# Optimization experiments

Hardware: AMD Instinct MI355X
Metric: run time of the kernel (lower is better)

## Reference

```python
import jax, jax.numpy as jnp
import numpy as np

B, LQ, LK, D, H = 2, 1024, 1024, 1024, 16
DH = D // H


def setup_inputs() -> dict:
    key = jax.random.key(0)
    ks = jax.random.split(key, 14)
    s = 1.0 / np.sqrt(D)
    inp = {
        "q": jax.random.normal(ks[0], (B, LQ, D), jnp.float32),
        "k": jax.random.normal(ks[1], (B, LK, D), jnp.float32),
        "v": jax.random.normal(ks[2], (B, LK, D), jnp.float32),
        "Wq": jax.random.normal(ks[3], (D, D), jnp.float32) * s,
        "bq": jnp.zeros((D,), jnp.float32),
        "Wk": jax.random.normal(ks[4], (D, D), jnp.float32) * s,
        "bk": jnp.zeros((D,), jnp.float32),
        "Wv": jax.random.normal(ks[5], (D, D), jnp.float32) * s,
        "bv": jnp.zeros((D,), jnp.float32),
        "Wo": jax.random.normal(ks[6], (D, D), jnp.float32) * s,
        "bo": jnp.zeros((D,), jnp.float32),
        "logits_bias": jax.random.normal(ks[7], (B, LQ, LK), jnp.float32),
        "key_padding_mask": jax.random.randint(ks[8], (B, LK), 0, 2) > 0,
    }
    return inp


def _split_heads(x):
    b, l, _ = x.shape
    return x.reshape(b, l, H, DH).transpose(0, 2, 1, 3)  # [B,H,L,DH]


def reference(q, k, v, Wq, bq, Wk, bk, Wv, bv, Wo, bo, logits_bias, key_padding_mask):
    qh = _split_heads(q @ Wq.T + bq)  # [B,H,Lq,DH]
    kh = _split_heads(k @ Wk.T + bk)  # [B,H,Lk,DH]
    vh = _split_heads(v @ Wv.T + bv)  # [B,H,Lk,DH]

    neg = jnp.finfo(qh.dtype).min
    # attn_mask = logits_bias broadcast over heads, masked_fill at padded keys
    attn_mask = jnp.where(key_padding_mask[:, None, None, :],
                          neg, logits_bias[:, None, :, :])  # [B,1,Lq,Lk]

    scale = 1.0 / np.sqrt(DH)
    scores = jnp.einsum('bhqd,bhkd->bhqk', qh, kh) * scale + attn_mask
    probs = jax.nn.softmax(scores, axis=-1)
    out = jnp.einsum('bhqk,bhkd->bhqd', probs, vh)  # [B,H,Lq,DH]
    out = out.transpose(0, 2, 1, 3).reshape(q.shape[0], q.shape[1], D)
    return out @ Wo.T + bo
```

## Files before the change

kernel.cpp:

```cpp
#include <hip/hip_runtime.h>


typedef _Float16 half8 __attribute__((ext_vector_type(8)));
typedef _Float16 half4_t __attribute__((ext_vector_type(4)));
typedef __fp16 fp16x2 __attribute__((ext_vector_type(2)));
typedef float f32x4 __attribute__((ext_vector_type(4)));
typedef unsigned int u32;

#define MFMA16(a, b, c) __builtin_amdgcn_mfma_f32_16x16x32_f16((a), (b), (c), 0, 0, 0)

#define WAITCNT_VM(n) asm volatile("s_waitcnt vmcnt(" #n ")" ::: "memory")
#define WAITCNT_LGKM0() asm volatile("s_waitcnt lgkmcnt(0)" ::: "memory")
#define RAW_BARRIER() asm volatile("s_barrier" ::: "memory")
#define EXP2F(x) __builtin_amdgcn_exp2f(x)

__device__ __forceinline__ void gload16(const void* g, void* l) {
  __builtin_amdgcn_global_load_lds(
      (const __attribute__((address_space(1))) unsigned int*)g,
      (__attribute__((address_space(3))) unsigned int*)l, 16, 0, 0);
}

__device__ __forceinline__ half8 frag_ld(const _Float16* t, int row, int ck) {
  return *(const half8*)(t + row * 64 + (((ck ^ (row & 7)) << 3)));
}

__global__ __launch_bounds__(256) void cvt_f32_f16(
    const float* __restrict__ q, const float* __restrict__ k, const float* __restrict__ v,
    const float* __restrict__ Wq, const float* __restrict__ Wk,
    const float* __restrict__ Wv, const float* __restrict__ Wo,
    _Float16* __restrict__ q16, _Float16* __restrict__ k16, _Float16* __restrict__ v16,
    _Float16* __restrict__ w16) {
  const int y = blockIdx.y;
  const float* s;
  _Float16* d;
  const size_t M = (size_t)1024 * 1024;
  int x = blockIdx.x;
  switch (y) {
    case 0: s = q;  d = q16; break;
    case 1: s = k;  d = k16; break;
    case 2: s = v;  d = v16; break;
    case 3: if (x < 512) { s = Wq; d = w16; } else { s = Wk; d = w16 + M; x -= 512; } break;
    default: if (x < 512) { s = Wv; d = w16 + 2 * M; } else { s = Wo; d = w16 + 3 * M; x -= 512; } break;
  }
  const size_t i = ((size_t)x * 256 + threadIdx.x) * 8;
  const float4 a = *(const float4*)(s + i);
  const float4 bvv = *(const float4*)(s + i + 4);
  half8 h;
  h[0] = (_Float16)a.x; h[1] = (_Float16)a.y; h[2] = (_Float16)a.z; h[3] = (_Float16)a.w;
  h[4] = (_Float16)bvv.x; h[5] = (_Float16)bvv.y; h[6] = (_Float16)bvv.z; h[7] = (_Float16)bvv.w;
  *(half8*)(d + i) = h;
}

__global__ __launch_bounds__(256, 2) void mmp_big(
    const _Float16* __restrict__ Aq, const _Float16* __restrict__ Ak,
    const _Float16* __restrict__ Av, const _Float16* __restrict__ W16,
    const float* __restrict__ c0, const float* __restrict__ c1,
    const float* __restrict__ c2, _Float16* __restrict__ Dq,
    _Float16* __restrict__ Dk, _Float16* __restrict__ Dvt) {
  __shared__ __align__(16) _Float16 lds[32768];

  const int tid = threadIdx.x;
  const int wv = tid >> 6, ln = tid & 63;
  const int quad = ln >> 4, col = ln & 15;
  const int wm = wv >> 1, wn = wv & 1;
  const int id = blockIdx.x;
  const int xcd = id & 7, idx = id >> 3;
  const int z = idx % 3;
  const int sub = idx / 3;
  const int n0 = ((xcd & 3) * 2 + (sub & 1)) * 128;
  const int m0 = ((xcd >> 2) * 8 + (sub >> 1)) * 128;
  const bool swapped = (z < 2);

  const _Float16* A = (z == 0) ? Aq : (z == 1) ? Ak : Av;
  const _Float16* Bw = W16 + (size_t)z * 1024 * 1024;
  const float* bias = (z == 0) ? c0 : (z == 1) ? c1 : c2;

  auto stage = [&](int buf, int k0) {
#pragma unroll
    for (int j = 0; j < 8; ++j) {
      const int ci = j * 256 + tid;
      const _Float16* src;
      if (ci < 1024) {
        const int row = ci >> 3, lc = (ci & 7) ^ (row & 7);
        src = A + (size_t)(m0 + row) * 1024 + k0 + lc * 8;
      } else {
        const int di = ci - 1024;
        const int row = di >> 3, lc = (di & 7) ^ (row & 7);
        src = Bw + (size_t)(n0 + row) * 1024 + k0 + lc * 8;
      }
      gload16(src, lds + buf * 16384 + (j * 256 + wv * 64) * 8);
    }
  };

  const f32x4 zero4 = {0.f, 0.f, 0.f, 0.f};
  f32x4 acc[4][4];
#pragma unroll
  for (int i = 0; i < 4; ++i)
#pragma unroll
    for (int j = 0; j < 4; ++j) acc[i][j] = zero4;

  auto kstep = [&](const _Float16* As, const _Float16* Bs) {
    half8 af0[4], bf0[4], af1[4], bf1[4];
#pragma unroll
    for (int mi = 0; mi < 4; ++mi) af0[mi] = frag_ld(As, wm * 64 + mi * 16 + col, quad);
#pragma unroll
    for (int ni = 0; ni < 4; ++ni) bf0[ni] = frag_ld(Bs, wn * 64 + ni * 16 + col, quad);
#pragma unroll
    for (int mi = 0; mi < 4; ++mi) af1[mi] = frag_ld(As, wm * 64 + mi * 16 + col, 4 + quad);
#pragma unroll
    for (int ni = 0; ni < 4; ++ni) bf1[ni] = frag_ld(Bs, wn * 64 + ni * 16 + col, 4 + quad);
    WAITCNT_LGKM0();
    RAW_BARRIER();
    if (swapped) {
#pragma unroll
      for (int ni = 0; ni < 4; ++ni)
#pragma unroll
        for (int mi = 0; mi < 4; ++mi)
          acc[ni][mi] = MFMA16(bf0[ni], af0[mi], acc[ni][mi]);
#pragma unroll
      for (int ni = 0; ni < 4; ++ni)
#pragma unroll
        for (int mi = 0; mi < 4; ++mi)
          acc[ni][mi] = MFMA16(bf1[ni], af1[mi], acc[ni][mi]);
    } else {
#pragma unroll
      for (int mi = 0; mi < 4; ++mi)
#pragma unroll
        for (int ni = 0; ni < 4; ++ni)
          acc[mi][ni] = MFMA16(af0[mi], bf0[ni], acc[mi][ni]);
#pragma unroll
      for (int mi = 0; mi < 4; ++mi)
#pragma unroll
        for (int ni = 0; ni < 4; ++ni)
          acc[mi][ni] = MFMA16(af1[mi], bf1[ni], acc[mi][ni]);
    }
  };

  stage(0, 0);
  for (int i = 0; i < 15; ++i) {
    stage((i + 1) & 1, (i + 1) * 64);
    WAITCNT_VM(8);
    RAW_BARRIER();
    kstep(lds + (i & 1) * 16384, lds + (i & 1) * 16384 + 8192);
  }
  WAITCNT_VM(0);
  RAW_BARRIER();
  kstep(lds + 16384, lds + 16384 + 8192);

  if (swapped) {
    float4 bv4[4];
#pragma unroll
    for (int ni = 0; ni < 4; ++ni)
      bv4[ni] = *(const float4*)&bias[n0 + wn * 64 + ni * 16 + quad * 4];
    _Float16* D = z ? Dk : Dq;
#pragma unroll
    for (int ni = 0; ni < 4; ++ni) {
      const int n_g = n0 + wn * 64 + ni * 16 + quad * 4;
      const int h = n_g >> 6, dh = n_g & 63;
#pragma unroll
      for (int mi = 0; mi < 4; ++mi) {
        const int m_g = m0 + wm * 64 + mi * 16 + col;
        const int b = m_g >> 10, l = m_g & 1023;
        half4_t st;
        st[0] = (_Float16)(acc[ni][mi][0] + bv4[ni].x);
        st[1] = (_Float16)(acc[ni][mi][1] + bv4[ni].y);
        st[2] = (_Float16)(acc[ni][mi][2] + bv4[ni].z);
        st[3] = (_Float16)(acc[ni][mi][3] + bv4[ni].w);
        *(half4_t*)&D[((size_t)((b * 16 + h) * 1024) + l) * 64 + dh] = st;
      }
    }
  } else {
    float bv[4];
#pragma unroll
    for (int ni = 0; ni < 4; ++ni) bv[ni] = bias[n0 + wn * 64 + ni * 16 + col];
    __syncthreads();
    _Float16* Ct = lds;
#pragma unroll
    for (int mi = 0; mi < 4; ++mi) {
      const int ml = wm * 64 + mi * 16 + quad * 4;
#pragma unroll
      for (int ni = 0; ni < 4; ++ni) {
        const int nl = wn * 64 + ni * 16 + col;
        half4_t h;
#pragma unroll
        for (int r = 0; r < 4; ++r) h[r] = (_Float16)(acc[mi][ni][r] + bv[ni]);
        *(half4_t*)(Ct + (size_t)nl * 136 + ml) = h;
      }
    }
    __syncthreads();
#pragma unroll
    for (int it = 0; it < 8; ++it) {
      const int ci = it * 256 + tid;
      const int n = ci >> 4;
      const int mc = (ci & 15) * 8;
      const half8 hv = *(const half8*)(Ct + (size_t)n * 136 + mc);
      const int n_g = n0 + n;
      const int h = n_g >> 6, dh = n_g & 63;
      const int m_g = m0 + mc;
      const int b = m_g >> 10, l = m_g & 1023;
      *(half8*)(Dvt + ((size_t)((b * 16 + h) * 64 + dh)) * 1024 + l) = hv;
    }
  }
}

__global__ __launch_bounds__(256) void mmp_final(
    const _Float16* __restrict__ A, const _Float16* __restrict__ Bw,
    const float* __restrict__ bias, float* __restrict__ Df) {
  __shared__ __align__(16) _Float16 lds[24576];

  const int tid = threadIdx.x;
  const int wv = tid >> 6, ln = tid & 63;
  const int quad = ln >> 4, col = ln & 15;
  const int wm = wv >> 1, wn = wv & 1;
  const int id = blockIdx.x;
  const int xcd = id & 7, idx = id >> 3;
  const int n0 = ((xcd & 1) * 4 + (idx & 3)) * 128;
  const int m0 = ((xcd >> 1) * 8 + (idx >> 2)) * 64;

  auto stage = [&](int buf, int k0) {
#pragma unroll
    for (int j = 0; j < 6; ++j) {
      const int ci = j * 256 + tid;
      const _Float16* src;
      if (ci < 512) {
        const int row = ci >> 3, lc = (ci & 7) ^ (row & 7);
        src = A + (size_t)(m0 + row) * 1024 + k0 + lc * 8;
      } else {
        const int di = ci - 512;
        const int row = di >> 3, lc = (di & 7) ^ (row & 7);
        src = Bw + (size_t)(n0 + row) * 1024 + k0 + lc * 8;
      }
      gload16(src, lds + buf * 12288 + (j * 256 + wv * 64) * 8);
    }
  };

  const f32x4 zero4 = {0.f, 0.f, 0.f, 0.f};
  f32x4 acc[4][2];
#pragma unroll
  for (int i = 0; i < 4; ++i)
#pragma unroll
    for (int j = 0; j < 2; ++j) acc[i][j] = zero4;

  auto kstep = [&](const _Float16* As, const _Float16* Bs) {
    half8 af[2][2], bf[2][4];
#pragma unroll
    for (int kk = 0; kk < 2; ++kk) {
#pragma unroll
      for (int mi = 0; mi < 2; ++mi)
        af[kk][mi] = frag_ld(As, wm * 32 + mi * 16 + col, kk * 4 + quad);
#pragma unroll
      for (int ni = 0; ni < 4; ++ni)
        bf[kk][ni] = frag_ld(Bs, wn * 64 + ni * 16 + col, kk * 4 + quad);
    }
    WAITCNT_LGKM0();
    RAW_BARRIER();
#pragma unroll
    for (int kk = 0; kk < 2; ++kk)
#pragma unroll
      for (int ni = 0; ni < 4; ++ni)
#pragma unroll
        for (int mi = 0; mi < 2; ++mi)
          acc[ni][mi] = MFMA16(bf[kk][ni], af[kk][mi], acc[ni][mi]);
  };

  stage(0, 0);
  for (int i = 0; i < 15; ++i) {
    stage((i + 1) & 1, (i + 1) * 64);
    WAITCNT_VM(6);
    RAW_BARRIER();
    kstep(lds + (i & 1) * 12288, lds + (i & 1) * 12288 + 4096);
  }
  WAITCNT_VM(0);
  RAW_BARRIER();
  kstep(lds + 12288, lds + 12288 + 4096);

  float4 bv4[4];
#pragma unroll
  for (int ni = 0; ni < 4; ++ni)
    bv4[ni] = *(const float4*)&bias[n0 + wn * 64 + ni * 16 + quad * 4];
#pragma unroll
  for (int ni = 0; ni < 4; ++ni) {
    const int n_g = n0 + wn * 64 + ni * 16 + quad * 4;
#pragma unroll
    for (int mi = 0; mi < 2; ++mi) {
      const int m_g = m0 + wm * 32 + mi * 16 + col;
      float4 st;
      st.x = acc[ni][mi][0] + bv4[ni].x;
      st.y = acc[ni][mi][1] + bv4[ni].y;
      st.z = acc[ni][mi][2] + bv4[ni].z;
      st.w = acc[ni][mi][3] + bv4[ni].w;
      *(float4*)&Df[(size_t)m_g * 1024 + n_g] = st;
    }
  }
}

__global__ __launch_bounds__(512, 4) void attn(
    const _Float16* __restrict__ Qh, const _Float16* __restrict__ Kh,
    const _Float16* __restrict__ Vt, const float* __restrict__ biasL,
    const int* __restrict__ kpm, _Float16* __restrict__ AO) {
  __shared__ __align__(16) _Float16 KV[3 * 8192];

  const int tid = threadIdx.x;
  const int wv = tid >> 6, ln = tid & 63;
  const int quad = ln >> 4, col = ln & 15;
  const int qsub = wv >> 1, khalf = wv & 1;
  const int fid = blockIdx.x;
  const int xcd = fid & 7, g = fid >> 3;
  const int bh = (xcd << 2) | (g >> 4);
  const int q0 = (g & 15) * 64;
  const int b = bh >> 4, hh = bh & 15;
  const int qg = q0 + qsub * 16 + col;

  const _Float16* Qp = Qh + ((size_t)bh * 1024 + qg) * 64;
  const half8 bq0 = *(const half8*)(Qp + quad * 8);
  const half8 bq1 = *(const half8*)(Qp + 32 + quad * 8);
  WAITCNT_VM(0);

  const float* biasRow = biasL + ((size_t)(b * 1024 + qg)) * 1024;
  const int* kpmRow = kpm + b * 1024;

  auto stageKV = [&](int buf, int it) {
    const int koff = it * 64;
#pragma unroll
    for (int j = 0; j < 2; ++j) {
      const int ci = j * 512 + tid;
      const void* src;
      if (ci < 512) {
        const int row = ci >> 3, lc = (ci & 7) ^ (row & 7);
        src = Kh + ((size_t)bh * 1024 + koff + row) * 64 + lc * 8;
      } else {
        const int di = ci - 512;
        const int row = di >> 3, lc = (di & 7) ^ (row & 7);
        src = Vt + ((size_t)bh * 64 + row) * 1024 + koff + lc * 8;
      }
      gload16(src, KV + buf * 8192 + (j * 512 + wv * 64) * 8);
    }
  };
  auto loadBias = [&](int it, f32x4* bb, int4* mk) {
    const int koff = it * 64 + khalf * 32;
#pragma unroll
    for (int mi = 0; mi < 2; ++mi) {
      const int kg = koff + mi * 16 + quad * 4;
      bb[mi] = *(const f32x4*)&biasRow[kg];
      mk[mi] = *(const int4*)&kpmRow[kg];
    }
  };

  const f32x4 zero4 = {0.f, 0.f, 0.f, 0.f};
  f32x4 o[4];
#pragma unroll
  for (int ni = 0; ni < 4; ++ni) o[ni] = zero4;
  float l_i = 0.f;

  auto pk = [](float a, float bb) -> u32 {
    union { fp16x2 h; u32 u; } cv;
    cv.h = __builtin_amdgcn_cvt_pkrtz(a, bb);
    return cv.u;
  };

  auto compute = [&](int buf, const f32x4* bb, const int4* mk) {
    const _Float16* Ks = KV + buf * 8192;
    const _Float16* Vs = Ks + 4096;
    f32x4 s[2];
#pragma unroll
    for (int mi = 0; mi < 2; ++mi) {
      f32x4 a4 = zero4;
      a4 = MFMA16(frag_ld(Ks, khalf * 32 + mi * 16 + col, quad), bq0, a4);
      a4 = MFMA16(frag_ld(Ks, khalf * 32 + mi * 16 + col, 4 + quad), bq1, a4);
      s[mi] = a4;
    }
#pragma unroll
    for (int mi = 0; mi < 2; ++mi) {
      const int* mp = (const int*)&mk[mi];
#pragma unroll
      for (int r = 0; r < 4; ++r) {
        const float sv = s[mi][r] * 0.18033688f + (bb[mi][r] * 1.44269504f - 8.f);
        const float p = mp[r] ? 0.f : EXP2F(sv);
        s[mi][r] = p;
        l_i += p;
      }
    }
    const u32 X0 = pk(s[0][0], s[0][1]), X1 = pk(s[0][2], s[0][3]);
    const u32 Y0 = pk(s[1][0], s[1][1]), Y1 = pk(s[1][2], s[1][3]);
    const u32 tX0 = __shfl_xor(X0, 16), tX1 = __shfl_xor(X1, 16);
    const u32 tY0 = __shfl_xor(Y0, 16), tY1 = __shfl_xor(Y1, 16);
    const bool e = (quad & 1) == 0;
    const u32 L0 = e ? X0 : tX0, L1 = e ? X1 : tX1, L2 = e ? tX0 : X0, L3 = e ? tX1 : X1;
    const u32 H0 = e ? Y0 : tY0, H1 = e ? Y1 : tY1, H2 = e ? tY0 : Y0, H3 = e ? tY1 : Y1;
    const bool lo2 = quad < 2;
    const u32 W0 = lo2 ? H0 : L0, W1 = lo2 ? H1 : L1, W2 = lo2 ? H2 : L2, W3 = lo2 ? H3 : L3;
    const u32 R0 = __shfl_xor(W0, 32), R1 = __shfl_xor(W1, 32);
    const u32 R2 = __shfl_xor(W2, 32), R3 = __shfl_xor(W3, 32);
    const bool mid = (quad == 1) || (quad == 2);
    union { u32 u[4]; half8 h; } pf;
    pf.u[0] = mid ? R0 : (lo2 ? L0 : H0);
    pf.u[1] = mid ? R1 : (lo2 ? L1 : H1);
    pf.u[2] = mid ? R2 : (lo2 ? L2 : H2);
    pf.u[3] = mid ? R3 : (lo2 ? L3 : H3);
#pragma unroll
    for (int ni = 0; ni < 4; ++ni)
      o[ni] = MFMA16(frag_ld(Vs, ni * 16 + col, khalf * 4 + quad), pf.h, o[ni]);
  };

  f32x4 bbA[2], bbB[2];
  int4 mkA[2], mkB[2];
  stageKV(0, 0);
  loadBias(0, bbA, mkA);
#pragma unroll 3
  for (int i = 0; i < 15; ++i) {
    stageKV((i + 1) % 3, i + 1);
    loadBias(i + 1, bbB, mkB);
    WAITCNT_VM(6);
    WAITCNT_LGKM0();
    RAW_BARRIER();
    compute(i % 3, bbA, mkA);
    bbA[0] = bbB[0]; bbA[1] = bbB[1];
    mkA[0] = mkB[0]; mkA[1] = mkB[1];
  }
  WAITCNT_VM(0);
  WAITCNT_LGKM0();
  RAW_BARRIER();
  compute(0, bbA, mkA);

  l_i += __shfl_xor(l_i, 16);
  l_i += __shfl_xor(l_i, 32);

  __syncthreads();
  f32x4* Ox = (f32x4*)&KV[0];
  float* MlS = (float*)&KV[8192];
  if (khalf == 1) {
#pragma unroll
    for (int ni = 0; ni < 4; ++ni) Ox[(qsub * 4 + ni) * 64 + ln] = o[ni];
    MlS[qsub * 64 + ln] = l_i;
  }
  __syncthreads();
  if (khalf == 0) {
    const float l2 = MlS[qsub * 64 + ln];
    const float inv = 1.0f / (l_i + l2);
#pragma unroll
    for (int ni = 0; ni < 4; ++ni) {
      const f32x4 o2 = Ox[(qsub * 4 + ni) * 64 + ln];
      half4_t h;
#pragma unroll
      for (int r = 0; r < 4; ++r)
        h[r] = (_Float16)((o[ni][r] + o2[r]) * inv);
      *(half4_t*)&AO[((size_t)(b * 1024 + qg)) * 1024 + hh * 64 + ni * 16 + quad * 4] = h;
    }
  }
}

extern "C" void kernel_launch(void* const* d_in, const int* in_sizes, int n_in,
                              void* d_out, int out_size, void* d_ws, size_t ws_size,
                              hipStream_t stream) {
  (void)in_sizes; (void)n_in; (void)out_size; (void)ws_size;
  const float* q = (const float*)d_in[0];
  const float* k = (const float*)d_in[1];
  const float* v = (const float*)d_in[2];
  const float* Wq = (const float*)d_in[3];
  const float* bq = (const float*)d_in[4];
  const float* Wk = (const float*)d_in[5];
  const float* bk = (const float*)d_in[6];
  const float* Wv = (const float*)d_in[7];
  const float* bv = (const float*)d_in[8];
  const float* Wo = (const float*)d_in[9];
  const float* bo = (const float*)d_in[10];
  const float* lb = (const float*)d_in[11];
  const int* kpm = (const int*)d_in[12];
  float* out = (float*)d_out;

  const size_t NT = (size_t)2 * 1024 * 1024;
  _Float16* q16 = (_Float16*)d_ws;
  _Float16* k16 = q16 + NT;
  _Float16* v16 = k16 + NT;
  _Float16* Qh = v16 + NT;
  _Float16* Kh = Qh + NT;
  _Float16* Vt = Kh + NT;
  _Float16* w16 = Vt + NT;
  _Float16* AO = q16;

  cvt_f32_f16<<<dim3(1024, 5), 256, 0, stream>>>(q, k, v, Wq, Wk, Wv, Wo,
                                                 q16, k16, v16, w16);
  mmp_big<<<dim3(384), 256, 0, stream>>>(q16, k16, v16, w16, bq, bk, bv,
                                         Qh, Kh, Vt);
  attn<<<dim3(512), 512, 0, stream>>>(Qh, Kh, Vt, lb, kpm, AO);
  mmp_final<<<dim3(256), 256, 0, stream>>>(AO, w16 + 3 * NT / 2, bo, out);
}
```

Measured before the change: 168.0 us.

## Fuse all four stages into one persistent kernel with grid barriers

Merges conversion, QKV projection, attention and output projection into a single 512-block persistent kernel separated by atomic-counter grid barriers, removing three kernel launch gaps. The attention stage is restructured from 512-thread blocks with a K-split across wave pairs to 256-thread blocks where each wave handles all 64 keys per step, dropping the LDS cross-wave reduction. It adds a memset and spin-wait barriers, lowers attention parallelism per block, and relies on all 512 blocks being co-resident, which risks deadlock if they are not.

Result: slower. 499.3 us (+197.1%).

```diff
diff --git a/kernel.cpp b/kernel.cpp
--- a/kernel.cpp
+++ b/kernel.cpp
@@ -24,427 +24,428 @@
   return *(const half8*)(t + row * 64 + (((ck ^ (row & 7)) << 3)));
 }
 
-__global__ __launch_bounds__(256) void cvt_f32_f16(
+__device__ __forceinline__ void grid_barrier(u32* bar, u32 nb) {
+  __threadfence();
+  __syncthreads();
+  if (threadIdx.x == 0) {
+    const u32 g = atomicAdd(bar + 1, 0u);
+    if (atomicAdd(bar, 1u) == nb - 1) {
+      atomicAdd(bar + 1, 1u);
+    } else {
+      while (atomicAdd(bar + 1, 0u) == g) __builtin_amdgcn_s_sleep(2);
+    }
+  }
+  __syncthreads();
+  __threadfence();
+}
+
+__global__ __launch_bounds__(256, 2) void fused(
     const float* __restrict__ q, const float* __restrict__ k, const float* __restrict__ v,
     const float* __restrict__ Wq, const float* __restrict__ Wk,
     const float* __restrict__ Wv, const float* __restrict__ Wo,
+    const float* __restrict__ biasL, const int* __restrict__ kpm,
+    const float* __restrict__ bq, const float* __restrict__ bk,
+    const float* __restrict__ bv, const float* __restrict__ bo,
     _Float16* __restrict__ q16, _Float16* __restrict__ k16, _Float16* __restrict__ v16,
-    _Float16* __restrict__ w16) {
-  const int y = blockIdx.y;
-  const float* s;
-  _Float16* d;
-  const size_t M = (size_t)1024 * 1024;
-  int x = blockIdx.x;
-  switch (y) {
-    case 0: s = q;  d = q16; break;
-    case 1: s = k;  d = k16; break;
-    case 2: s = v;  d = v16; break;
-    case 3: if (x < 512) { s = Wq; d = w16; } else { s = Wk; d = w16 + M; x -= 512; } break;
-    default: if (x < 512) { s = Wv; d = w16 + 2 * M; } else { s = Wo; d = w16 + 3 * M; x -= 512; } break;
-  }
-  const size_t i = ((size_t)x * 256 + threadIdx.x) * 8;
-  const float4 a = *(const float4*)(s + i);
-  const float4 bvv = *(const float4*)(s + i + 4);
-  half8 h;
-  h[0] = (_Float16)a.x; h[1] = (_Float16)a.y; h[2] = (_Float16)a.z; h[3] = (_Float16)a.w;
-  h[4] = (_Float16)bvv.x; h[5] = (_Float16)bvv.y; h[6] = (_Float16)bvv.z; h[7] = (_Float16)bvv.w;
-  *(half8*)(d + i) = h;
-}
-
-__global__ __launch_bounds__(256, 2) void mmp_big(
-    const _Float16* __restrict__ Aq, const _Float16* __restrict__ Ak,
-    const _Float16* __restrict__ Av, const _Float16* __restrict__ W16,
-    const float* __restrict__ c0, const float* __restrict__ c1,
-    const float* __restrict__ c2, _Float16* __restrict__ Dq,
-    _Float16* __restrict__ Dk, _Float16* __restrict__ Dvt) {
+    _Float16* __restrict__ w16, _Float16* __restrict__ Qh, _Float16* __restrict__ Kh,
+    _Float16* __restrict__ Vt, _Float16* __restrict__ AO, float* __restrict__ out,
+    u32* __restrict__ bars) {
   __shared__ __align__(16) _Float16 lds[32768];
 
   const int tid = threadIdx.x;
+  const int bid = blockIdx.x;
   const int wv = tid >> 6, ln = tid & 63;
   const int quad = ln >> 4, col = ln & 15;
-  const int wm = wv >> 1, wn = wv & 1;
-  const int id = blockIdx.x;
-  const int xcd = id & 7, idx = id >> 3;
-  const int z = idx % 3;
-  const int sub = idx / 3;
-  const int n0 = ((xcd & 3) * 2 + (sub & 1)) * 128;
-  const int m0 = ((xcd >> 2) * 8 + (sub >> 1)) * 128;
-  const bool swapped = (z < 2);
-
-  const _Float16* A = (z == 0) ? Aq : (z == 1) ? Ak : Av;
-  const _Float16* Bw = W16 + (size_t)z * 1024 * 1024;
-  const float* bias = (z == 0) ? c0 : (z == 1) ? c1 : c2;
-
-  auto stage = [&](int buf, int k0) {
-#pragma unroll
-    for (int j = 0; j < 8; ++j) {
-      const int ci = j * 256 + tid;
-      const _Float16* src;
-      if (ci < 1024) {
-        const int row = ci >> 3, lc = (ci & 7) ^ (row & 7);
-        src = A + (size_t)(m0 + row) * 1024 + k0 + lc * 8;
+  const f32x4 zero4 = {0.f, 0.f, 0.f, 0.f};
+
+  {
+    const size_t Mel = 1048576;
+    const int tidg = bid * 256 + tid;
+#pragma unroll
+    for (int it = 0; it < 10; ++it) {
+      const size_t e0 = ((size_t)it * 131072 + tidg) * 8;
+      const float* s;
+      _Float16* d;
+      if (e0 < 2 * Mel)      { s = q + e0;             d = q16 + e0; }
+      else if (e0 < 4 * Mel) { s = k + (e0 - 2 * Mel); d = k16 + (e0 - 2 * Mel); }
+      else if (e0 < 6 * Mel) { s = v + (e0 - 4 * Mel); d = v16 + (e0 - 4 * Mel); }
+      else {
+        const size_t w = e0 - 6 * Mel;
+        const int wi = (int)(w >> 20);
+        const float* ws = (wi == 0) ? Wq : (wi == 1) ? Wk : (wi == 2) ? Wv : Wo;
+        s = ws + (w & (Mel - 1));
+        d = w16 + w;
+      }
+      const float4 a = *(const float4*)s;
+      const float4 b2 = *(const float4*)(s + 4);
+      half8 h;
+      h[0] = (_Float16)a.x;  h[1] = (_Float16)a.y;  h[2] = (_Float16)a.z;  h[3] = (_Float16)a.w;
+      h[4] = (_Float16)b2.x; h[5] = (_Float16)b2.y; h[6] = (_Float16)b2.z; h[7] = (_Float16)b2.w;
+      *(half8*)d = h;
+    }
+  }
+  WAITCNT_VM(0);
+  grid_barrier(bars + 0, 512);
+
+  if (bid < 384) {
+    const int xcd = bid & 7, idx = bid >> 3;
+    const int z = idx % 3;
+    const int sub = idx / 3;
+    const int n0 = ((xcd & 3) * 2 + (sub & 1)) * 128;
+    const int m0 = ((xcd >> 2) * 8 + (sub >> 1)) * 128;
+    const bool swapped = (z < 2);
+    const int wm = wv >> 1, wn = wv & 1;
+
+    const _Float16* A = (z == 0) ? q16 : (z == 1) ? k16 : v16;
+    const _Float16* Bw = w16 + (size_t)z * 1024 * 1024;
+    const float* bias = (z == 0) ? bq : (z == 1) ? bk : bv;
+
+    auto stage = [&](int buf, int k0) {
+#pragma unroll
+      for (int j = 0; j < 8; ++j) {
+        const int ci = j * 256 + tid;
+        const _Float16* src;
+        if (ci < 1024) {
+          const int row = ci >> 3, lc = (ci & 7) ^ (row & 7);
+          src = A + (size_t)(m0 + row) * 1024 + k0 + lc * 8;
+        } else {
+          const int di = ci - 1024;
+          const int row = di >> 3, lc = (di & 7) ^ (row & 7);
+          src = Bw + (size_t)(n0 + row) * 1024 + k0 + lc * 8;
+        }
+        gload16(src, lds + buf * 16384 + (j * 256 + wv * 64) * 8);
+      }
+    };
+
+    f32x4 acc[4][4];
+#pragma unroll
+    for (int i = 0; i < 4; ++i)
+#pragma unroll
+      for (int j = 0; j < 4; ++j) acc[i][j] = zero4;
+
+    auto kstep = [&](const _Float16* As, const _Float16* Bs) {
+      half8 af0[4], bf0[4], af1[4], bf1[4];
+#pragma unroll
+      for (int mi = 0; mi < 4; ++mi) af0[mi] = frag_ld(As, wm * 64 + mi * 16 + col, quad);
+#pragma unroll
+      for (int ni = 0; ni < 4; ++ni) bf0[ni] = frag_ld(Bs, wn * 64 + ni * 16 + col, quad);
+#pragma unroll
+      for (int mi = 0; mi < 4; ++mi) af1[mi] = frag_ld(As, wm * 64 + mi * 16 + col, 4 + quad);
+#pragma unroll
+      for (int ni = 0; ni < 4; ++ni) bf1[ni] = frag_ld(Bs, wn * 64 + ni * 16 + col, 4 + quad);
+      WAITCNT_LGKM0();
+      RAW_BARRIER();
+      if (swapped) {
+#pragma unroll
+        for (int ni = 0; ni < 4; ++ni)
+#pragma unroll
+          for (int mi = 0; mi < 4; ++mi)
+            acc[ni][mi] = MFMA16(bf0[ni], af0[mi], acc[ni][mi]);
+#pragma unroll
+        for (int ni = 0; ni < 4; ++ni)
+#pragma unroll
+          for (int mi = 0; mi < 4; ++mi)
+            acc[ni][mi] = MFMA16(bf1[ni], af1[mi], acc[ni][mi]);
       } else {
-        const int di = ci - 1024;
-        const int row = di >> 3, lc = (di & 7) ^ (row & 7);
-        src = Bw + (size_t)(n0 + row) * 1024 + k0 + lc * 8;
-      }
-      gload16(src, lds + buf * 16384 + (j * 256 + wv * 64) * 8);
-    }
-  };
-
-  const f32x4 zero4 = {0.f, 0.f, 0.f, 0.f};
-  f32x4 acc[4][4];
-#pragma unroll
-  for (int i = 0; i < 4; ++i)
-#pragma unroll
-    for (int j = 0; j < 4; ++j) acc[i][j] = zero4;
-
-  auto kstep = [&](const _Float16* As, const _Float16* Bs) {
-    half8 af0[4], bf0[4], af1[4], bf1[4];
-#pragma unroll
-    for (int mi = 0; mi < 4; ++mi) af0[mi] = frag_ld(As, wm * 64 + mi * 16 + col, quad);
-#pragma unroll
-    for (int ni = 0; ni < 4; ++ni) bf0[ni] = frag_ld(Bs, wn * 64 + ni * 16 + col, quad);
-#pragma unroll
-    for (int mi = 0; mi < 4; ++mi) af1[mi] = frag_ld(As, wm * 64 + mi * 16 + col, 4 + quad);
-#pragma unroll
-    for (int ni = 0; ni < 4; ++ni) bf1[ni] = frag_ld(Bs, wn * 64 + ni * 16 + col, 4 + quad);
+#pragma unroll
+        for (int mi = 0; mi < 4; ++mi)
+#pragma unroll
+          for (int ni = 0; ni < 4; ++ni)
+            acc[mi][ni] = MFMA16(af0[mi], bf0[ni], acc[mi][ni]);
+#pragma unroll
+        for (int mi = 0; mi < 4; ++mi)
+#pragma unroll
+          for (int ni = 0; ni < 4; ++ni)
+            acc[mi][ni] = MFMA16(af1[mi], bf1[ni], acc[mi][ni]);
+      }
+    };
+
+    stage(0, 0);
+    for (int i = 0; i < 15; ++i) {
+      stage((i + 1) & 1, (i + 1) * 64);
+      WAITCNT_VM(8);
+      RAW_BARRIER();
+      kstep(lds + (i & 1) * 16384, lds + (i & 1) * 16384 + 8192);
+    }
+    WAITCNT_VM(0);
+    RAW_BARRIER();
+    kstep(lds + 16384, lds + 16384 + 8192);
+
+    if (swapped) {
+      float4 bv4[4];
+#pragma unroll
+      for (int ni = 0; ni < 4; ++ni)
+        bv4[ni] = *(const float4*)&bias[n0 + wn * 64 + ni * 16 + quad * 4];
+      _Float16* D = z ? Kh : Qh;
+#pragma unroll
+      for (int ni = 0; ni < 4; ++ni) {
+        const int n_g = n0 + wn * 64 + ni * 16 + quad * 4;
+        const int h = n_g >> 6, dh = n_g & 63;
+#pragma unroll
+        for (int mi = 0; mi < 4; ++mi) {
+          const int m_g = m0 + wm * 64 + mi * 16 + col;
+          const int b = m_g >> 10, l = m_g & 1023;
+          half4_t st;
+          st[0] = (_Float16)(acc[ni][mi][0] + bv4[ni].x);
+          st[1] = (_Float16)(acc[ni][mi][1] + bv4[ni].y);
+          st[2] = (_Float16)(acc[ni][mi][2] + bv4[ni].z);
+          st[3] = (_Float16)(acc[ni][mi][3] + bv4[ni].w);
+          *(half4_t*)&D[((size_t)((b * 16 + h) * 1024) + l) * 64 + dh] = st;
+        }
+      }
+    } else {
+      float bvv[4];
+#pragma unroll
+      for (int ni = 0; ni < 4; ++ni) bvv[ni] = bias[n0 + wn * 64 + ni * 16 + col];
+      __syncthreads();
+      _Float16* Ct = lds;
+#pragma unroll
+      for (int mi = 0; mi < 4; ++mi) {
+        const int ml = wm * 64 + mi * 16 + quad * 4;
+#pragma unroll
+        for (int ni = 0; ni < 4; ++ni) {
+          const int nl = wn * 64 + ni * 16 + col;
+          half4_t h;
+#pragma unroll
+          for (int r = 0; r < 4; ++r) h[r] = (_Float16)(acc[mi][ni][r] + bvv[ni]);
+          *(half4_t*)(Ct + (size_t)nl * 136 + ml) = h;
+        }
+      }
+      __syncthreads();
+#pragma unroll
+      for (int it = 0; it < 8; ++it) {
+        const int ci = it * 256 + tid;
+        const int n = ci >> 4;
+        const int mc = (ci & 15) * 8;
+        const half8 hv = *(const half8*)(Ct + (size_t)n * 136 + mc);
+        const int n_g = n0 + n;
+        const int h = n_g >> 6, dh = n_g & 63;
+        const int m_g = m0 + mc;
+        const int b = m_g >> 10, l = m_g & 1023;
+        *(half8*)(Vt + ((size_t)((b * 16 + h) * 64 + dh)) * 1024 + l) = hv;
+      }
+    }
+  }
+  grid_barrier(bars + 2, 512);
+
+  {
+    const int xcd = bid & 7, g = bid >> 3;
+    const int bh = (xcd << 2) | (g >> 4);
+    const int q0 = (g & 15) * 64;
+    const int b = bh >> 4, hh = bh & 15;
+    const int qsub = wv;
+    const int qg = q0 + qsub * 16 + col;
+
+    const _Float16* Qp = Qh + ((size_t)bh * 1024 + qg) * 64;
+    const half8 bq0 = *(const half8*)(Qp + quad * 8);
+    const half8 bq1 = *(const half8*)(Qp + 32 + quad * 8);
+    WAITCNT_VM(0);
+
+    const float* biasRow = biasL + ((size_t)(b * 1024 + qg)) * 1024;
+    const int* kpmRow = kpm + b * 1024;
+
+    auto stageKV = [&](int buf, int it) {
+      const int koff = it * 64;
+#pragma unroll
+      for (int j = 0; j < 4; ++j) {
+        const int ci = j * 256 + tid;
+        const void* src;
+        if (ci < 512) {
+          const int row = ci >> 3, lc = (ci & 7) ^ (row & 7);
+          src = Kh + ((size_t)bh * 1024 + koff + row) * 64 + lc * 8;
+        } else {
+          const int di = ci - 512;
+          const int row = di >> 3, lc = (di & 7) ^ (row & 7);
+          src = Vt + ((size_t)bh * 64 + row) * 1024 + koff + lc * 8;
+        }
+        gload16(src, lds + buf * 8192 + (j * 256 + wv * 64) * 8);
+      }
+    };
+    auto loadBias = [&](int it, f32x4* bb, int4* mk) {
+      const int koff = it * 64;
+#pragma unroll
+      for (int mi = 0; mi < 4; ++mi) {
+        const int kg = koff + mi * 16 + quad * 4;
+        bb[mi] = *(const f32x4*)&biasRow[kg];
+        mk[mi] = *(const int4*)&kpmRow[kg];
+      }
+    };
+
+    f32x4 o[4];
+#pragma unroll
+    for (int ni = 0; ni < 4; ++ni) o[ni] = zero4;
+    float l_i = 0.f;
+
+    auto pk = [](float a, float bb) -> u32 {
+      union { fp16x2 h; u32 u; } cv;
+      cv.h = __builtin_amdgcn_cvt_pkrtz(a, bb);
+      return cv.u;
+    };
+    auto shuffle32 = [&](u32 X0, u32 X1, u32 Y0, u32 Y1, u32* pu) {
+      const u32 tX0 = __shfl_xor(X0, 16), tX1 = __shfl_xor(X1, 16);
+      const u32 tY0 = __shfl_xor(Y0, 16), tY1 = __shfl_xor(Y1, 16);
+      const bool e = (quad & 1) == 0;
+      const u32 L0 = e ? X0 : tX0, L1 = e ? X1 : tX1, L2 = e ? tX0 : X0, L3 = e ? tX1 : X1;
+      const u32 H0 = e ? Y0 : tY0, H1 = e ? Y1 : tY1, H2 = e ? tY0 : Y0, H3 = e ? tY1 : Y1;
+      const bool lo2 = quad < 2;
+      const u32 W0 = lo2 ? H0 : L0, W1 = lo2 ? H1 : L1, W2 = lo2 ? H2 : L2, W3 = lo2 ? H3 : L3;
+      const u32 R0 = __shfl_xor(W0, 32), R1 = __shfl_xor(W1, 32);
+      const u32 R2 = __shfl_xor(W2, 32), R3 = __shfl_xor(W3, 32);
+      const bool mid = (quad == 1) || (quad == 2);
+      pu[0] = mid ? R0 : (lo2 ? L0 : H0);
+      pu[1] = mid ? R1 : (lo2 ? L1 : H1);
+      pu[2] = mid ? R2 : (lo2 ? L2 : H2);
+      pu[3] = mid ? R3 : (lo2 ? L3 : H3);
+    };
+
+    auto compute = [&](int buf, const f32x4* bb, const int4* mk) {
+      const _Float16* Ks = lds + buf * 8192;
+      const _Float16* Vs = Ks + 4096;
+      f32x4 s[4];
+#pragma unroll
+      for (int mi = 0; mi < 4; ++mi) {
+        f32x4 a4 = zero4;
+        a4 = MFMA16(frag_ld(Ks, mi * 16 + col, quad), bq0, a4);
+        a4 = MFMA16(frag_ld(Ks, mi * 16 + col, 4 + quad), bq1, a4);
+        s[mi] = a4;
+      }
+#pragma unroll
+      for (int mi = 0; mi < 4; ++mi) {
+        const int* mp = (const int*)&mk[mi];
+#pragma unroll
+        for (int r = 0; r < 4; ++r) {
+          const float sv = s[mi][r] * 0.18033688f + (bb[mi][r] * 1.44269504f - 8.f);
+          const float p = mp[r] ? 0.f : EXP2F(sv);
+          s[mi][r] = p;
+          l_i += p;
+        }
+      }
+      union { u32 u[4]; half8 h; } pf0, pf1;
+      shuffle32(pk(s[0][0], s[0][1]), pk(s[0][2], s[0][3]),
+                pk(s[1][0], s[1][1]), pk(s[1][2], s[1][3]), pf0.u);
+      shuffle32(pk(s[2][0], s[2][1]), pk(s[2][2], s[2][3]),
+                pk(s[3][0], s[3][1]), pk(s[3][2], s[3][3]), pf1.u);
+#pragma unroll
+      for (int ni = 0; ni < 4; ++ni) {
+        o[ni] = MFMA16(frag_ld(Vs, ni * 16 + col, quad), pf0.h, o[ni]);
+        o[ni] = MFMA16(frag_ld(Vs, ni * 16 + col, 4 + quad), pf1.h, o[ni]);
+      }
+    };
+
+    f32x4 bbA[4], bbB[4];
+    int4 mkA[4], mkB[4];
+    stageKV(0, 0);
+    loadBias(0, bbA, mkA);
+#pragma unroll 3
+    for (int i = 0; i < 15; ++i) {
+      stageKV((i + 1) % 3, i + 1);
+      loadBias(i + 1, bbB, mkB);
+      WAITCNT_VM(12);
+      WAITCNT_LGKM0();
+      RAW_BARRIER();
+      compute(i % 3, bbA, mkA);
+#pragma unroll
+      for (int x2 = 0; x2 < 4; ++x2) { bbA[x2] = bbB[x2]; mkA[x2] = mkB[x2]; }
+    }
+    WAITCNT_VM(0);
     WAITCNT_LGKM0();
     RAW_BARRIER();
-    if (swapped) {
-#pragma unroll
-      for (int ni = 0; ni < 4; ++ni)
-#pragma unroll
-        for (int mi = 0; mi < 4; ++mi)
-          acc[ni][mi] = MFMA16(bf0[ni], af0[mi], acc[ni][mi]);
-#pragma unroll
-      for (int ni = 0; ni < 4; ++ni)
-#pragma unroll
-        for (int mi = 0; mi < 4; ++mi)
-          acc[ni][mi] = MFMA16(bf1[ni], af1[mi], acc[ni][mi]);
-    } else {
-#pragma unroll
-      for (int mi = 0; mi < 4; ++mi)
+    compute(0, bbA, mkA);
+
+    l_i += __shfl_xor(l_i, 16);
+    l_i += __shfl_xor(l_i, 32);
+    const float inv = 1.0f / l_i;
+#pragma unroll
+    for (int ni = 0; ni < 4; ++ni) {
+      half4_t h;
+#pragma unroll
+      for (int r = 0; r < 4; ++r) h[r] = (_Float16)(o[ni][r] * inv);
+      *(half4_t*)&AO[((size_t)(b * 1024 + qg)) * 1024 + hh * 64 + ni * 16 + quad * 4] = h;
+    }
+  }
+  grid_barrier(bars + 4, 512);
+
+  if (bid < 256) {
+    const int xcd = bid & 7, idx = bid >> 3;
+    const int n0 = ((xcd & 1) * 4 + (idx & 3)) * 128;
+    const int m0 = ((xcd >> 1) * 8 + (idx >> 2)) * 64;
+    const int wm = wv >> 1, wn = wv & 1;
+    const _Float16* A = AO;
+    const _Float16* Bw = w16 + (size_t)3 * 1024 * 1024;
+
+    auto stage = [&](int buf, int k0) {
+#pragma unroll
+      for (int j = 0; j < 6; ++j) {
+        const int ci = j * 256 + tid;
+        const _Float16* src;
+        if (ci < 512) {
+          const int row = ci >> 3, lc = (ci & 7) ^ (row & 7);
+          src = A + (size_t)(m0 + row) * 1024 + k0 + lc * 8;
+        } else {
+          const int di = ci - 512;
+          const int row = di >> 3, lc = (di & 7) ^ (row & 7);
+          src = Bw + (size_t)(n0 + row) * 1024 + k0 + lc * 8;
+        }
+        gload16(src, lds + buf * 12288 + (j * 256 + wv * 64) * 8);
+      }
+    };
+
+    f32x4 acc[4][2];
+#pragma unroll
+    for (int i = 0; i < 4; ++i)
+#pragma unroll
+      for (int j = 0; j < 2; ++j) acc[i][j] = zero4;
+
+    auto kstep = [&](const _Float16* As, const _Float16* Bs) {
+      half8 af[2][2], bf[2][4];
+#pragma unroll
+      for (int kk = 0; kk < 2; ++kk) {
+#pragma unroll
+        for (int mi = 0; mi < 2; ++mi)
+          af[kk][mi] = frag_ld(As, wm * 32 + mi * 16 + col, kk * 4 + quad);
 #pragma unroll
         for (int ni = 0; ni < 4; ++ni)
-          acc[mi][ni] = MFMA16(af0[mi], bf0[ni], acc[mi][ni]);
-#pragma unroll
-      for (int mi = 0; mi < 4; ++mi)
+          bf[kk][ni] = frag_ld(Bs, wn * 64 + ni * 16 + col, kk * 4 + quad);
+      }
+      WAITCNT_LGKM0();
+      RAW_BARRIER();
+#pragma unroll
+      for (int kk = 0; kk < 2; ++kk)
 #pragma unroll
         for (int ni = 0; ni < 4; ++ni)
-          acc[mi][ni] = MFMA16(af1[mi], bf1[ni], acc[mi][ni]);
-    }
-  };
-
-  stage(0, 0);
-  for (int i = 0; i < 15; ++i) {
-    stage((i + 1) & 1, (i + 1) * 64);
-    WAITCNT_VM(8);
+#pragma unroll
+          for (int mi = 0; mi < 2; ++mi)
+            acc[ni][mi] = MFMA16(bf[kk][ni], af[kk][mi], acc[ni][mi]);
+    };
+
+    stage(0, 0);
+    for (int i = 0; i < 15; ++i) {
+      stage((i + 1) & 1, (i + 1) * 64);
+      WAITCNT_VM(6);
+      RAW_BARRIER();
+      kstep(lds + (i & 1) * 12288, lds + (i & 1) * 12288 + 4096);
+    }
+    WAITCNT_VM(0);
     RAW_BARRIER();
-    kstep(lds + (i & 1) * 16384, lds + (i & 1) * 16384 + 8192);
-  }
-  WAITCNT_VM(0);
-  RAW_BARRIER();
-  kstep(lds + 16384, lds + 16384 + 8192);
-
-  if (swapped) {
+    kstep(lds + 12288, lds + 12288 + 4096);
+
     float4 bv4[4];
 #pragma unroll
     for (int ni = 0; ni < 4; ++ni)
-      bv4[ni] = *(const float4*)&bias[n0 + wn * 64 + ni * 16 + quad * 4];
-    _Float16* D = z ? Dk : Dq;
+      bv4[ni] = *(const float4*)&bo[n0 + wn * 64 + ni * 16 + quad * 4];
 #pragma unroll
     for (int ni = 0; ni < 4; ++ni) {
       const int n_g = n0 + wn * 64 + ni * 16 + quad * 4;
-      const int h = n_g >> 6, dh = n_g & 63;
-#pragma unroll
-      for (int mi = 0; mi < 4; ++mi) {
-        const int m_g = m0 + wm * 64 + mi * 16 + col;
-        const int b = m_g >> 10, l = m_g & 1023;
-        half4_t st;
-        st[0] = (_Float16)(acc[ni][mi][0] + bv4[ni].x);
-        st[1] = (_Float16)(acc[ni][mi][1] + bv4[ni].y);
-        st[2] = (_Float16)(acc[ni][mi][2] + bv4[ni].z);
-        st[3] = (_Float16)(acc[ni][mi][3] + bv4[ni].w);
-        *(half4_t*)&D[((size_t)((b * 16 + h) * 1024) + l) * 64 + dh] = st;
-      }
-    }
-  } else {
-    float bv[4];
-#pragma unroll
-    for (int ni = 0; ni < 4; ++ni) bv[ni] = bias[n0 + wn * 64 + ni * 16 + col];
-    __syncthreads();
-    _Float16* Ct = lds;
-#pragma unroll
-    for (int mi = 0; mi < 4; ++mi) {
-      const int ml = wm * 64 + mi * 16 + quad * 4;
-#pragma unroll
-      for (int ni = 0; ni < 4; ++ni) {
-        const int nl = wn * 64 + ni * 16 + col;
-        half4_t h;
-#pragma unroll
-        for (int r = 0; r < 4; ++r) h[r] = (_Float16)(acc[mi][ni][r] + bv[ni]);
-        *(half4_t*)(Ct + (size_t)nl * 136 + ml) = h;
-      }
-    }
-    __syncthreads();
-#pragma unroll
-    for (int it = 0; it < 8; ++it) {
-      const int ci = it * 256 + tid;
-      const int n = ci >> 4;
-      const int mc = (ci & 15) * 8;
-      const half8 hv = *(const half8*)(Ct + (size_t)n * 136 + mc);
-      const int n_g = n0 + n;
-      const int h = n_g >> 6, dh = n_g & 63;
-      const int m_g = m0 + mc;
-      const int b = m_g >> 10, l = m_g & 1023;
-      *(half8*)(Dvt + ((size_t)((b * 16 + h) * 64 + dh)) * 1024 + l) = hv;
-    }
-  }
-}
-
-__global__ __launch_bounds__(256) void mmp_final(
-    const _Float16* __restrict__ A, const _Float16* __restrict__ Bw,
-    const float* __restrict__ bias, float* __restrict__ Df) {
-  __shared__ __align__(16) _Float16 lds[24576];
-
-  const int tid = threadIdx.x;
-  const int wv = tid >> 6, ln = tid & 63;
-  const int quad = ln >> 4, col = ln & 15;
-  const int wm = wv >> 1, wn = wv & 1;
-  const int id = blockIdx.x;
-  const int xcd = id & 7, idx = id >> 3;
-  const int n0 = ((xcd & 1) * 4 + (idx & 3)) * 128;
-  const int m0 = ((xcd >> 1) * 8 + (idx >> 2)) * 64;
-
-  auto stage = [&](int buf, int k0) {
-#pragma unroll
-    for (int j = 0; j < 6; ++j) {
-      const int ci = j * 256 + tid;
-      const _Float16* src;
-      if (ci < 512) {
-        const int row = ci >> 3, lc = (ci & 7) ^ (row & 7);
-        src = A + (size_t)(m0 + row) * 1024 + k0 + lc * 8;
-      } else {
-        const int di = ci - 512;
-        const int row = di >> 3, lc = (di & 7) ^ (row & 7);
-        src = Bw + (size_t)(n0 + row) * 1024 + k0 + lc * 8;
-      }
-      gload16(src, lds + buf * 12288 + (j * 256 + wv * 64) * 8);
-    }
-  };
-
-  const f32x4 zero4 = {0.f, 0.f, 0.f, 0.f};
-  f32x4 acc[4][2];
-#pragma unroll
-  for (int i = 0; i < 4; ++i)
-#pragma unroll
-    for (int j = 0; j < 2; ++j) acc[i][j] = zero4;
-
-  auto kstep = [&](const _Float16* As, const _Float16* Bs) {
-    half8 af[2][2], bf[2][4];
-#pragma unroll
-    for (int kk = 0; kk < 2; ++kk) {
-#pragma unroll
-      for (int mi = 0; mi < 2; ++mi)
-        af[kk][mi] = frag_ld(As, wm * 32 + mi * 16 + col, kk * 4 + quad);
-#pragma unroll
-      for (int ni = 0; ni < 4; ++ni)
-        bf[kk][ni] = frag_ld(Bs, wn * 64 + ni * 16 + col, kk * 4 + quad);
-    }
-    WAITCNT_LGKM0();
-    RAW_BARRIER();
-#pragma unroll
-    for (int kk = 0; kk < 2; ++kk)
-#pragma unroll
-      for (int ni = 0; ni < 4; ++ni)
-#pragma unroll
-        for (int mi = 0; mi < 2; ++mi)
-          acc[ni][mi] = MFMA16(bf[kk][ni], af[kk][mi], acc[ni][mi]);
-  };
-
-  stage(0, 0);
-  for (int i = 0; i < 15; ++i) {
-    stage((i + 1) & 1, (i + 1) * 64);
-    WAITCNT_VM(6);
-    RAW_BARRIER();
-    kstep(lds + (i & 1) * 12288, lds + (i & 1) * 12288 + 4096);
-  }
-  WAITCNT_VM(0);
-  RAW_BARRIER();
-  kstep(lds + 12288, lds + 12288 + 4096);
-
-  float4 bv4[4];
-#pragma unroll
-  for (int ni = 0; ni < 4; ++ni)
-    bv4[ni] = *(const float4*)&bias[n0 + wn * 64 + ni * 16 + quad * 4];
-#pragma unroll
-  for (int ni = 0; ni < 4; ++ni) {
-    const int n_g = n0 + wn * 64 + ni * 16 + quad * 4;
-#pragma unroll
-    for (int mi = 0; mi < 2; ++mi) {
-      const int m_g = m0 + wm * 32 + mi * 16 + col;
-      float4 st;
-      st.x = acc[ni][mi][0] + bv4[ni].x;
-      st.y = acc[ni][mi][1] + bv4[ni].y;
-      st.z = acc[ni][mi][2] + bv4[ni].z;
-      st.w = acc[ni][mi][3] + bv4[ni].w;
-      *(float4*)&Df[(size_t)m_g * 1024 + n_g] = st;
-    }
-  }
-}
-
-__global__ __launch_bounds__(512, 4) void attn(
-    const _Float16* __restrict__ Qh, const _Float16* __restrict__ Kh,
-    const _Float16* __restrict__ Vt, const float* __restrict__ biasL,
-    const int* __restrict__ kpm, _Float16* __restrict__ AO) {
-  __shared__ __align__(16) _Float16 KV[3 * 8192];
-
-  const int tid = threadIdx.x;
-  const int wv = tid >> 6, ln = tid & 63;
-  const int quad = ln >> 4, col = ln & 15;
-  const int qsub = wv >> 1, khalf = wv & 1;
-  const int fid = blockIdx.x;
-  const int xcd = fid & 7, g = fid >> 3;
-  const int bh = (xcd << 2) | (g >> 4);
-  const int q0 = (g & 15) * 64;
-  const int b = bh >> 4, hh = bh & 15;
-  const int qg = q0 + qsub * 16 + col;
-
-  const _Float16* Qp = Qh + ((size_t)bh * 1024 + qg) * 64;
-  const half8 bq0 = *(const half8*)(Qp + quad * 8);
-  const half8 bq1 = *(const half8*)(Qp + 32 + quad * 8);
-  WAITCNT_VM(0);
-
-  const float* biasRow = biasL + ((size_t)(b * 1024 + qg)) * 1024;
-  const int* kpmRow = kpm + b * 1024;
-
-  auto stageKV = [&](int buf, int it) {
-    const int koff = it * 64;
-#pragma unroll
-    for (int j = 0; j < 2; ++j) {
-      const int ci = j * 512 + tid;
-      const void* src;
-      if (ci < 512) {
-        const int row = ci >> 3, lc = (ci & 7) ^ (row & 7);
-        src = Kh + ((size_t)bh * 1024 + koff + row) * 64 + lc * 8;
-      } else {
-        const int di = ci - 512;
-        const int row = di >> 3, lc = (di & 7) ^ (row & 7);
-        src = Vt + ((size_t)bh * 64 + row) * 1024 + koff + lc * 8;
-      }
-      gload16(src, KV + buf * 8192 + (j * 512 + wv * 64) * 8);
-    }
-  };
-  auto loadBias = [&](int it, f32x4* bb, int4* mk) {
-    const int koff = it * 64 + khalf * 32;
-#pragma unroll
-    for (int mi = 0; mi < 2; ++mi) {
-      const int kg = koff + mi * 16 + quad * 4;
-      bb[mi] = *(const f32x4*)&biasRow[kg];
-      mk[mi] = *(const int4*)&kpmRow[kg];
-    }
-  };
-
-  const f32x4 zero4 = {0.f, 0.f, 0.f, 0.f};
-  f32x4 o[4];
-#pragma unroll
-  for (int ni = 0; ni < 4; ++ni) o[ni] = zero4;
-  float l_i = 0.f;
-
-  auto pk = [](float a, float bb) -> u32 {
-    union { fp16x2 h; u32 u; } cv;
-    cv.h = __builtin_amdgcn_cvt_pkrtz(a, bb);
-    return cv.u;
-  };
-
-  auto compute = [&](int buf, const f32x4* bb, const int4* mk) {
-    const _Float16* Ks = KV + buf * 8192;
-    const _Float16* Vs = Ks + 4096;
-    f32x4 s[2];
-#pragma unroll
-    for (int mi = 0; mi < 2; ++mi) {
-      f32x4 a4 = zero4;
-      a4 = MFMA16(frag_ld(Ks, khalf * 32 + mi * 16 + col, quad), bq0, a4);
-      a4 = MFMA16(frag_ld(Ks, khalf * 32 + mi * 16 + col, 4 + quad), bq1, a4);
-      s[mi] = a4;
-    }
-#pragma unroll
-    for (int mi = 0; mi < 2; ++mi) {
-      const int* mp = (const int*)&mk[mi];
-#pragma unroll
-      for (int r = 0; r < 4; ++r) {
-        const float sv = s[mi][r] * 0.18033688f + (bb[mi][r] * 1.44269504f - 8.f);
-        const float p = mp[r] ? 0.f : EXP2F(sv);
-        s[mi][r] = p;
-        l_i += p;
-      }
-    }
-    const u32 X0 = pk(s[0][0], s[0][1]), X1 = pk(s[0][2], s[0][3]);
-    const u32 Y0 = pk(s[1][0], s[1][1]), Y1 = pk(s[1][2], s[1][3]);
-    const u32 tX0 = __shfl_xor(X0, 16), tX1 = __shfl_xor(X1, 16);
-    const u32 tY0 = __shfl_xor(Y0, 16), tY1 = __shfl_xor(Y1, 16);
-    const bool e = (quad & 1) == 0;
-    const u32 L0 = e ? X0 : tX0, L1 = e ? X1 : tX1, L2 = e ? tX0 : X0, L3 = e ? tX1 : X1;
-    const u32 H0 = e ? Y0 : tY0, H1 = e ? Y1 : tY1, H2 = e ? tY0 : Y0, H3 = e ? tY1 : Y1;
-    const bool lo2 = quad < 2;
-    const u32 W0 = lo2 ? H0 : L0, W1 = lo2 ? H1 : L1, W2 = lo2 ? H2 : L2, W3 = lo2 ? H3 : L3;
-    const u32 R0 = __shfl_xor(W0, 32), R1 = __shfl_xor(W1, 32);
-    const u32 R2 = __shfl_xor(W2, 32), R3 = __shfl_xor(W3, 32);
-    const bool mid = (quad == 1) || (quad == 2);
-    union { u32 u[4]; half8 h; } pf;
-    pf.u[0] = mid ? R0 : (lo2 ? L0 : H0);
-    pf.u[1] = mid ? R1 : (lo2 ? L1 : H1);
-    pf.u[2] = mid ? R2 : (lo2 ? L2 : H2);
-    pf.u[3] = mid ? R3 : (lo2 ? L3 : H3);
-#pragma unroll
-    for (int ni = 0; ni < 4; ++ni)
-      o[ni] = MFMA16(frag_ld(Vs, ni * 16 + col, khalf * 4 + quad), pf.h, o[ni]);
-  };
-
-  f32x4 bbA[2], bbB[2];
-  int4 mkA[2], mkB[2];
-  stageKV(0, 0);
-  loadBias(0, bbA, mkA);
-#pragma unroll 3
-  for (int i = 0; i < 15; ++i) {
-    stageKV((i + 1) % 3, i + 1);
-    loadBias(i + 1, bbB, mkB);
-    WAITCNT_VM(6);
-    WAITCNT_LGKM0();
-    RAW_BARRIER();
-    compute(i % 3, bbA, mkA);
-    bbA[0] = bbB[0]; bbA[1] = bbB[1];
-    mkA[0] = mkB[0]; mkA[1] = mkB[1];
-  }
-  WAITCNT_VM(0);
-  WAITCNT_LGKM0();
-  RAW_BARRIER();
-  compute(0, bbA, mkA);
-
-  l_i += __shfl_xor(l_i, 16);
-  l_i += __shfl_xor(l_i, 32);
-
-  __syncthreads();
-  f32x4* Ox = (f32x4*)&KV[0];
-  float* MlS = (float*)&KV[8192];
-  if (khalf == 1) {
-#pragma unroll
-    for (int ni = 0; ni < 4; ++ni) Ox[(qsub * 4 + ni) * 64 + ln] = o[ni];
-    MlS[qsub * 64 + ln] = l_i;
-  }
-  __syncthreads();
-  if (khalf == 0) {
-    const float l2 = MlS[qsub * 64 + ln];
-    const float inv = 1.0f / (l_i + l2);
-#pragma unroll
-    for (int ni = 0; ni < 4; ++ni) {
-      const f32x4 o2 = Ox[(qsub * 4 + ni) * 64 + ln];
-      half4_t h;
-#pragma unroll
-      for (int r = 0; r < 4; ++r)
-        h[r] = (_Float16)((o[ni][r] + o2[r]) * inv);
-      *(half4_t*)&AO[((size_t)(b * 1024 + qg)) * 1024 + hh * 64 + ni * 16 + quad * 4] = h;
+#pragma unroll
+      for (int mi = 0; mi < 2; ++mi) {
+        const int m_g = m0 + wm * 32 + mi * 16 + col;
+        float4 st;
+        st.x = acc[ni][mi][0] + bv4[ni].x;
+        st.y = acc[ni][mi][1] + bv4[ni].y;
+        st.z = acc[ni][mi][2] + bv4[ni].z;
+        st.w = acc[ni][mi][3] + bv4[ni].w;
+        *(float4*)&out[(size_t)m_g * 1024 + n_g] = st;
+      }
     }
   }
 }
@@ -476,12 +477,11 @@
   _Float16* Kh = Qh + NT;
   _Float16* Vt = Kh + NT;
   _Float16* w16 = Vt + NT;
-  _Float16* AO = q16;
-
-  cvt_f32_f16<<<dim3(1024, 5), 256, 0, stream>>>(q, k, v, Wq, Wk, Wv, Wo,
-                                                 q16, k16, v16, w16);
-  mmp_big<<<dim3(384), 256, 0, stream>>>(q16, k16, v16, w16, bq, bk, bv,
-                                         Qh, Kh, Vt);
-  attn<<<dim3(512), 512, 0, stream>>>(Qh, Kh, Vt, lb, kpm, AO);
-  mmp_final<<<dim3(256), 256, 0, stream>>>(AO, w16 + 3 * NT / 2, bo, out);
+  _Float16* AO = w16 + 4 * (NT / 2);
+  u32* bars = (u32*)(AO + NT);
+
+  hipMemsetAsync(bars, 0, 64, stream);
+  fused<<<dim3(512), dim3(256), 0, stream>>>(
+      q, k, v, Wq, Wk, Wv, Wo, lb, kpm, bq, bk, bv, bo,
+      q16, k16, v16, w16, Qh, Kh, Vt, AO, out, bars);
 }
```
